# Kernel optimization log

Measured on AMD Instinct MI355X. Metric: run time of the kernel, lower is better.

## Reference

```python
import jax, jax.numpy as jnp
import numpy as np

N_NODES = 100000
N_EDGES = 1600000
IN_CH = 64
HID = 64
OUT_CH = 2
N_LAYERS = 3
NUM_GRAPHS = 2048
BN_EPS = 1e-5


def setup_inputs() -> dict:
    key = jax.random.key(0)
    ks = jax.random.split(key, 16)
    x = jax.random.normal(ks[0], (N_NODES, IN_CH), dtype=jnp.float32)
    edge_index = jax.random.randint(ks[1], (2, N_EDGES), 0, N_NODES, dtype=jnp.int32)
    batch = jnp.sort(jax.random.randint(ks[2], (N_NODES,), 0, NUM_GRAPHS, dtype=jnp.int32))
    s = 0.1  # weight scale
    inp = {
        "x": x,
        "edge_index": edge_index,
        "batch": batch,
        # stacked GINConv MLP params (in_ch == hidden so all layers share shapes)
        "convW1": jax.random.normal(ks[3], (N_LAYERS, IN_CH, HID), dtype=jnp.float32) * s,
        "convb1": jax.random.normal(ks[4], (N_LAYERS, HID), dtype=jnp.float32) * s,
        "bn_gamma": jnp.ones((N_LAYERS, HID), dtype=jnp.float32),
        "bn_beta": jnp.zeros((N_LAYERS, HID), dtype=jnp.float32),
        "bn_mean": jax.random.normal(ks[5], (N_LAYERS, HID), dtype=jnp.float32) * s,
        "bn_var": jax.random.uniform(ks[6], (N_LAYERS, HID), dtype=jnp.float32) + 0.5,
        "convW2": jax.random.normal(ks[7], (N_LAYERS, HID, HID), dtype=jnp.float32) * s,
        "convb2": jax.random.normal(ks[8], (N_LAYERS, HID), dtype=jnp.float32) * s,
        # final classifier MLP (norm=None, dropout=0.5 -> identity in eval)
        "mlpW1": jax.random.normal(ks[9], (HID, HID), dtype=jnp.float32) * s,
        "mlpb1": jax.random.normal(ks[10], (HID,), dtype=jnp.float32) * s,
        "mlpW2": jax.random.normal(ks[11], (HID, OUT_CH), dtype=jnp.float32) * s,
        "mlpb2": jax.random.normal(ks[12], (OUT_CH,), dtype=jnp.float32) * s,
    }
    return inp


def reference(x, edge_index, batch, convW1, convb1, bn_gamma, bn_beta, bn_mean,
              bn_var, convW2, convb2, mlpW1, mlpb1, mlpW2, mlpb2):
    N = x.shape[0]
    src, dst = edge_index[0], edge_index[1]
    for l in range(N_LAYERS):
        # GINConv, eps=0: h_i = MLP(x_i + sum_{j->i} x_j)
        agg = jax.ops.segment_sum(x[src], dst, num_segments=N)  # [N, C]
        h = x + agg
        # MLP: Linear -> BatchNorm(eval) -> ReLU -> Linear
        h = h @ convW1[l] + convb1[l]
        h = (h - bn_mean[l]) * jax.lax.rsqrt(bn_var[l] + BN_EPS) * bn_gamma[l] + bn_beta[l]
        h = jax.nn.relu(h)
        h = h @ convW2[l] + convb2[l]
        x = jax.nn.relu(h)  # .relu() after each conv in forward
    # global mean pool over graphs
    sums = jax.ops.segment_sum(x, batch, num_segments=NUM_GRAPHS)          # [G, H]
    counts = jax.ops.segment_sum(jnp.ones((N, 1), x.dtype), batch, num_segments=NUM_GRAPHS)
    pooled = sums / jnp.maximum(counts, 1.0)
    # final MLP: Linear -> ReLU -> (Dropout, identity in eval) -> Linear
    h = jax.nn.relu(pooled @ mlpW1 + mlpb1)
    logits = h @ mlpW2 + mlpb2
    return jax.nn.softmax(logits, axis=1)
```

## Files before the change

kernel.cpp:

```cpp
#include <hip/hip_runtime.h>

#define N_NODES   100000
#define N_EDGES   1600000
#define CH        64
#define N_LAYERS  3
#define NUM_GRAPHS 2048
#define BN_EPS    1e-5f
#define NSLICE    8
#define SLICE_SZ  12500

#define NP        100096
#define NBLK1     391
#define LDSTRIDE  65

__global__ __launch_bounds__(256) void hist_kernel(
    const int* __restrict__ dst, int* __restrict__ deg)
{
    int e = blockIdx.x * 256 + threadIdx.x;
    if (e < N_EDGES) atomicAdd(&deg[dst[e]], 1);
}

__global__ __launch_bounds__(256) void scan1_kernel(
    const int* __restrict__ deg, int* __restrict__ rowptr, int* __restrict__ blockSums)
{
    __shared__ int tmp[256];
    int t = threadIdx.x;
    int i = blockIdx.x * 256 + t;
    int v = (i < N_NODES) ? deg[i] : 0;
    tmp[t] = v;
    __syncthreads();
    for (int off = 1; off < 256; off <<= 1) {
        int a = (t >= off) ? tmp[t - off] : 0;
        __syncthreads();
        tmp[t] += a;
        __syncthreads();
    }
    if (i < N_NODES) rowptr[i] = tmp[t] - v;
    if (t == 255) blockSums[blockIdx.x] = tmp[255];
}

__global__ __launch_bounds__(512) void scan2_kernel(
    const int* __restrict__ blockSums, int* __restrict__ blockPrefix)
{
    __shared__ int tmp[512];
    int t = threadIdx.x;
    int v = (t < NBLK1) ? blockSums[t] : 0;
    tmp[t] = v;
    __syncthreads();
    for (int off = 1; off < 512; off <<= 1) {
        int a = (t >= off) ? tmp[t - off] : 0;
        __syncthreads();
        tmp[t] += a;
        __syncthreads();
    }
    if (t < NBLK1) blockPrefix[t] = tmp[t] - v;
}

__global__ __launch_bounds__(256) void scan3_kernel(
    int* __restrict__ rowptr, const int* __restrict__ blockPrefix)
{
    int i = blockIdx.x * 256 + threadIdx.x;
    if (i < N_NODES) rowptr[i] += blockPrefix[blockIdx.x];
}

__global__ __launch_bounds__(256) void scatter_edges_kernel(
    const int* __restrict__ src, const int* __restrict__ dst,
    int* __restrict__ rowptr, int* __restrict__ eidx)
{
    const int grp = blockIdx.x & (NSLICE - 1);
    const int ib  = blockIdx.x >> 3;
    const int nbx = gridDim.x >> 3;
    const int lo  = grp * SLICE_SZ;
    const int hi  = lo + SLICE_SZ;
    for (int e = ib * 256 + threadIdx.x; e < N_EDGES; e += nbx * 256) {
        int d = dst[e];
        if (d >= lo && d < hi) {
            int pos = atomicAdd(&rowptr[d], 1);
            eidx[pos] = src[e];
        }
    }
}

__global__ __launch_bounds__(256) void aggregate_kernel(
    const float* __restrict__ xin,
    const int*   __restrict__ rowptr, const int* __restrict__ deg,
    const int*   __restrict__ eidx,
    float*       __restrict__ h)
{
    int tid = blockIdx.x * 256 + threadIdx.x;
    int n  = tid >> 4;
    int cg = tid & 15;

    const float4* xv = (const float4*)xin;
    float4 acc = xv[(size_t)n * 16 + cg];

    int end = rowptr[n];
    int e   = end - deg[n];
    for (; e + 8 <= end; e += 8) {
        int s0 = eidx[e + 0], s1 = eidx[e + 1], s2 = eidx[e + 2], s3 = eidx[e + 3];
        int s4 = eidx[e + 4], s5 = eidx[e + 5], s6 = eidx[e + 6], s7 = eidx[e + 7];
        float4 a0 = xv[(size_t)s0 * 16 + cg];
        float4 a1 = xv[(size_t)s1 * 16 + cg];
        float4 a2 = xv[(size_t)s2 * 16 + cg];
        float4 a3 = xv[(size_t)s3 * 16 + cg];
        float4 a4 = xv[(size_t)s4 * 16 + cg];
        float4 a5 = xv[(size_t)s5 * 16 + cg];
        float4 a6 = xv[(size_t)s6 * 16 + cg];
        float4 a7 = xv[(size_t)s7 * 16 + cg];
        acc.x += a0.x; acc.y += a0.y; acc.z += a0.z; acc.w += a0.w;
        acc.x += a1.x; acc.y += a1.y; acc.z += a1.z; acc.w += a1.w;
        acc.x += a2.x; acc.y += a2.y; acc.z += a2.z; acc.w += a2.w;
        acc.x += a3.x; acc.y += a3.y; acc.z += a3.z; acc.w += a3.w;
        acc.x += a4.x; acc.y += a4.y; acc.z += a4.z; acc.w += a4.w;
        acc.x += a5.x; acc.y += a5.y; acc.z += a5.z; acc.w += a5.w;
        acc.x += a6.x; acc.y += a6.y; acc.z += a6.z; acc.w += a6.w;
        acc.x += a7.x; acc.y += a7.y; acc.z += a7.z; acc.w += a7.w;
    }
    for (; e + 4 <= end; e += 4) {
        int s0 = eidx[e + 0], s1 = eidx[e + 1], s2 = eidx[e + 2], s3 = eidx[e + 3];
        float4 a0 = xv[(size_t)s0 * 16 + cg];
        float4 a1 = xv[(size_t)s1 * 16 + cg];
        float4 a2 = xv[(size_t)s2 * 16 + cg];
        float4 a3 = xv[(size_t)s3 * 16 + cg];
        acc.x += a0.x; acc.y += a0.y; acc.z += a0.z; acc.w += a0.w;
        acc.x += a1.x; acc.y += a1.y; acc.z += a1.z; acc.w += a1.w;
        acc.x += a2.x; acc.y += a2.y; acc.z += a2.z; acc.w += a2.w;
        acc.x += a3.x; acc.y += a3.y; acc.z += a3.z; acc.w += a3.w;
    }
    for (; e < end; ++e) {
        float4 a = xv[(size_t)eidx[e] * 16 + cg];
        acc.x += a.x; acc.y += a.y; acc.z += a.z; acc.w += a.w;
    }
    ((float4*)h)[(size_t)n * 16 + cg] = acc;
}

__global__ __launch_bounds__(128) void mlp_kernel(
    const float* __restrict__ hin,
    const float* __restrict__ W1,   const float* __restrict__ b1,
    const float* __restrict__ gamma,const float* __restrict__ beta,
    const float* __restrict__ mean, const float* __restrict__ var,
    const float* __restrict__ W2,   const float* __restrict__ b2,
    float* __restrict__ xout)
{
    __shared__ float sbuf[2 * 64 * LDSTRIDE];

    const int lane = threadIdx.x & 63;
    const int wv   = threadIdx.x >> 6;
    const int gw   = blockIdx.x * 2 + wv;
    float* lds = sbuf + wv * (64 * LDSTRIDE);

    const long long base = (long long)gw * 64 * CH;
    const long long totF = (long long)N_NODES * CH;

    const float4* gin4 = (const float4*)(hin + base);
    for (int i = lane; i < 1024; i += 64) {
        int fo = i * 4;
        float4 v = make_float4(0.f, 0.f, 0.f, 0.f);
        if (base + fo + 3 < totF) v = gin4[i];
        int row = fo >> 6, col = fo & 63;
        float* p = lds + row * LDSTRIDE + col;
        p[0] = v.x; p[1] = v.y; p[2] = v.z; p[3] = v.w;
    }
    __syncthreads();

    float* myrow = lds + lane * LDSTRIDE;

    float a[CH];
    #pragma unroll
    for (int j = 0; j < CH; ++j) a[j] = b1[j];
    for (int k = 0; k < CH; ++k) {
        float hk = myrow[k];
        const float* wrow = W1 + k * CH;
        #pragma unroll
        for (int j = 0; j < CH; ++j)
            a[j] = fmaf(hk, wrow[j], a[j]);
    }

    #pragma unroll
    for (int j = 0; j < CH; ++j) {
        float sc = gamma[j] * rsqrtf(var[j] + BN_EPS);
        float sh = beta[j] - mean[j] * sc;
        myrow[j] = fmaxf(fmaf(a[j], sc, sh), 0.0f);
    }

    float c[CH];
    #pragma unroll
    for (int j = 0; j < CH; ++j) c[j] = b2[j];
    for (int k = 0; k < CH; ++k) {
        float tk = myrow[k];
        const float* wrow = W2 + k * CH;
        #pragma unroll
        for (int j = 0; j < CH; ++j)
            c[j] = fmaf(tk, wrow[j], c[j]);
    }

    #pragma unroll
    for (int j = 0; j < CH; ++j)
        myrow[j] = fmaxf(c[j], 0.0f);
    __syncthreads();

    float4* gout4 = (float4*)(xout + base);
    for (int i = lane; i < 1024; i += 64) {
        int fo = i * 4;
        if (base + fo + 3 < totF) {
            int row = fo >> 6, col = fo & 63;
            const float* p = lds + row * LDSTRIDE + col;
            gout4[i] = make_float4(p[0], p[1], p[2], p[3]);
        }
    }
}

__global__ __launch_bounds__(256) void pool_head_kernel(
    const float* __restrict__ x, const int* __restrict__ batch,
    const float* __restrict__ W1, const float* __restrict__ b1,
    const float* __restrict__ W2, const float* __restrict__ b2,
    float* __restrict__ out)
{
    __shared__ float w1[CH * CH];
    __shared__ float b1s[CH];
    __shared__ float w2s[CH * 2];

    for (int i = threadIdx.x; i < CH * CH; i += blockDim.x) w1[i] = W1[i];
    if (threadIdx.x < CH)     b1s[threadIdx.x] = b1[threadIdx.x];
    if (threadIdx.x < CH * 2) w2s[threadIdx.x] = W2[threadIdx.x];
    __syncthreads();

    const int lane = threadIdx.x & 63;
    const int g = blockIdx.x * (blockDim.x >> 6) + (threadIdx.x >> 6);
    if (g >= NUM_GRAPHS) return;

    int lo = 0, hi = N_NODES;
    while (lo < hi) { int mid = (lo + hi) >> 1; if (batch[mid] < g) lo = mid + 1; else hi = mid; }
    int start = lo;
    lo = start; hi = N_NODES;
    while (lo < hi) { int mid = (lo + hi) >> 1; if (batch[mid] < g + 1) lo = mid + 1; else hi = mid; }
    int end = lo;

    float s = 0.0f;
    for (int n = start; n < end; ++n) s += x[(size_t)n * CH + lane];
    int c = end - start;
    float p = s / (float)(c > 0 ? c : 1);

    float acc = b1s[lane];
    #pragma unroll
    for (int k = 0; k < CH; ++k)
        acc = fmaf(__shfl(p, k, 64), w1[k * CH + lane], acc);
    float h = fmaxf(acc, 0.0f);

    float l0 = h * w2s[lane * 2 + 0];
    float l1 = h * w2s[lane * 2 + 1];
    #pragma unroll
    for (int off = 32; off > 0; off >>= 1) {
        l0 += __shfl_xor(l0, off, 64);
        l1 += __shfl_xor(l1, off, 64);
    }
    if (lane == 0) {
        l0 += b2[0];
        l1 += b2[1];
        float m  = fmaxf(l0, l1);
        float e0 = expf(l0 - m), e1 = expf(l1 - m);
        float sm = e0 + e1;
        out[(size_t)g * 2 + 0] = e0 / sm;
        out[(size_t)g * 2 + 1] = e1 / sm;
    }
}

extern "C" void kernel_launch(void* const* d_in, const int* in_sizes, int n_in,
                              void* d_out, int out_size, void* d_ws, size_t ws_size,
                              hipStream_t stream)
{
    const float* x      = (const float*)d_in[0];
    const int*   ei     = (const int*)  d_in[1];
    const int*   src    = ei;
    const int*   dst    = ei + N_EDGES;
    const int*   batch  = (const int*)  d_in[2];
    const float* convW1 = (const float*)d_in[3];
    const float* convb1 = (const float*)d_in[4];
    const float* gamma  = (const float*)d_in[5];
    const float* beta   = (const float*)d_in[6];
    const float* mean   = (const float*)d_in[7];
    const float* var    = (const float*)d_in[8];
    const float* convW2 = (const float*)d_in[9];
    const float* convb2 = (const float*)d_in[10];
    const float* mlpW1  = (const float*)d_in[11];
    const float* mlpb1  = (const float*)d_in[12];
    const float* mlpW2  = (const float*)d_in[13];
    const float* mlpb2  = (const float*)d_in[14];
    float* out = (float*)d_out;

    int* deg         = (int*)d_ws;
    int* rowptr      = deg + NP;
    int* blockSums   = rowptr + NP;
    int* blockPrefix = blockSums + 512;
    int* eidx        = blockPrefix + 512;
    float* xA        = (float*)(eidx + N_EDGES);
    float* xB        = xA + (size_t)N_NODES * CH;

    hipMemsetAsync(deg, 0, NP * sizeof(int), stream);
    hist_kernel<<<(N_EDGES + 255) / 256, 256, 0, stream>>>(dst, deg);
    scan1_kernel<<<NBLK1, 256, 0, stream>>>(deg, rowptr, blockSums);
    scan2_kernel<<<1, 512, 0, stream>>>(blockSums, blockPrefix);
    scan3_kernel<<<NBLK1, 256, 0, stream>>>(rowptr, blockPrefix);
    scatter_edges_kernel<<<2048, 256, 0, stream>>>(src, dst, rowptr, eidx);

    const int aggGrid = (N_NODES * 16) / 256;
    const int mlpGrid = (N_NODES + 127) / 128;

    aggregate_kernel<<<aggGrid, 256, 0, stream>>>(x, rowptr, deg, eidx, xA);
    mlp_kernel<<<mlpGrid, 128, 0, stream>>>(xA,
        convW1, convb1, gamma, beta, mean, var, convW2, convb2, xA);
    aggregate_kernel<<<aggGrid, 256, 0, stream>>>(xA, rowptr, deg, eidx, xB);
    mlp_kernel<<<mlpGrid, 128, 0, stream>>>(xB,
        convW1 + CH*CH, convb1 + CH, gamma + CH, beta + CH, mean + CH, var + CH,
        convW2 + CH*CH, convb2 + CH, xB);
    aggregate_kernel<<<aggGrid, 256, 0, stream>>>(xB, rowptr, deg, eidx, xA);
    mlp_kernel<<<mlpGrid, 128, 0, stream>>>(xA,
        convW1 + 2*CH*CH, convb1 + 2*CH, gamma + 2*CH, beta + 2*CH, mean + 2*CH,
        var + 2*CH, convW2 + 2*CH*CH, convb2 + 2*CH, xA);

    pool_head_kernel<<<NUM_GRAPHS / 4, 256, 0, stream>>>(
        xA, batch, mlpW1, mlpb1, mlpW2, mlpb2, out);
}
```

Measured before the change: 602.1 us.

## Fuse neighbor aggregation with GIN MLP into one per-layer kernel

Merges the aggregate and MLP kernels into a single per-layer kernel. Each block gathers 64 nodes' aggregated features into LDS, then four waves each compute 16 output columns of both linear layers. This drops the global round trip of the aggregated buffer and one launch per layer, in exchange for more barriers and the MLP being split across waves. The edge scatter is also split into two launches over halves of the edge range, which may change atomic contention or ordering.

```diff
diff --git a/kernel.cpp b/kernel.cpp
--- a/kernel.cpp
+++ b/kernel.cpp
@@ -63,16 +63,17 @@
     if (i < N_NODES) rowptr[i] += blockPrefix[blockIdx.x];
 }
 
-__global__ __launch_bounds__(256) void scatter_edges_kernel(
+__global__ __launch_bounds__(256) void scatter_edges_half_kernel(
     const int* __restrict__ src, const int* __restrict__ dst,
-    int* __restrict__ rowptr, int* __restrict__ eidx)
+    int* __restrict__ rowptr, int* __restrict__ eidx,
+    int eBegin, int eEnd)
 {
     const int grp = blockIdx.x & (NSLICE - 1);
     const int ib  = blockIdx.x >> 3;
     const int nbx = gridDim.x >> 3;
     const int lo  = grp * SLICE_SZ;
     const int hi  = lo + SLICE_SZ;
-    for (int e = ib * 256 + threadIdx.x; e < N_EDGES; e += nbx * 256) {
+    for (int e = eBegin + ib * 256 + threadIdx.x; e < eEnd; e += nbx * 256) {
         int d = dst[e];
         if (d >= lo && d < hi) {
             int pos = atomicAdd(&rowptr[d], 1);
@@ -81,131 +82,130 @@
     }
 }
 
-__global__ __launch_bounds__(256) void aggregate_kernel(
+__global__ __launch_bounds__(256) void gin_layer_kernel(
     const float* __restrict__ xin,
     const int*   __restrict__ rowptr, const int* __restrict__ deg,
     const int*   __restrict__ eidx,
-    float*       __restrict__ h)
-{
-    int tid = blockIdx.x * 256 + threadIdx.x;
-    int n  = tid >> 4;
-    int cg = tid & 15;
-
-    const float4* xv = (const float4*)xin;
-    float4 acc = xv[(size_t)n * 16 + cg];
-
-    int end = rowptr[n];
-    int e   = end - deg[n];
-    for (; e + 8 <= end; e += 8) {
-        int s0 = eidx[e + 0], s1 = eidx[e + 1], s2 = eidx[e + 2], s3 = eidx[e + 3];
-        int s4 = eidx[e + 4], s5 = eidx[e + 5], s6 = eidx[e + 6], s7 = eidx[e + 7];
-        float4 a0 = xv[(size_t)s0 * 16 + cg];
-        float4 a1 = xv[(size_t)s1 * 16 + cg];
-        float4 a2 = xv[(size_t)s2 * 16 + cg];
-        float4 a3 = xv[(size_t)s3 * 16 + cg];
-        float4 a4 = xv[(size_t)s4 * 16 + cg];
-        float4 a5 = xv[(size_t)s5 * 16 + cg];
-        float4 a6 = xv[(size_t)s6 * 16 + cg];
-        float4 a7 = xv[(size_t)s7 * 16 + cg];
-        acc.x += a0.x; acc.y += a0.y; acc.z += a0.z; acc.w += a0.w;
-        acc.x += a1.x; acc.y += a1.y; acc.z += a1.z; acc.w += a1.w;
-        acc.x += a2.x; acc.y += a2.y; acc.z += a2.z; acc.w += a2.w;
-        acc.x += a3.x; acc.y += a3.y; acc.z += a3.z; acc.w += a3.w;
-        acc.x += a4.x; acc.y += a4.y; acc.z += a4.z; acc.w += a4.w;
-        acc.x += a5.x; acc.y += a5.y; acc.z += a5.z; acc.w += a5.w;
-        acc.x += a6.x; acc.y += a6.y; acc.z += a6.z; acc.w += a6.w;
-        acc.x += a7.x; acc.y += a7.y; acc.z += a7.z; acc.w += a7.w;
-    }
-    for (; e + 4 <= end; e += 4) {
-        int s0 = eidx[e + 0], s1 = eidx[e + 1], s2 = eidx[e + 2], s3 = eidx[e + 3];
-        float4 a0 = xv[(size_t)s0 * 16 + cg];
-        float4 a1 = xv[(size_t)s1 * 16 + cg];
-        float4 a2 = xv[(size_t)s2 * 16 + cg];
-        float4 a3 = xv[(size_t)s3 * 16 + cg];
-        acc.x += a0.x; acc.y += a0.y; acc.z += a0.z; acc.w += a0.w;
-        acc.x += a1.x; acc.y += a1.y; acc.z += a1.z; acc.w += a1.w;
-        acc.x += a2.x; acc.y += a2.y; acc.z += a2.z; acc.w += a2.w;
-        acc.x += a3.x; acc.y += a3.y; acc.z += a3.z; acc.w += a3.w;
-    }
-    for (; e < end; ++e) {
-        float4 a = xv[(size_t)eidx[e] * 16 + cg];
-        acc.x += a.x; acc.y += a.y; acc.z += a.z; acc.w += a.w;
-    }
-    ((float4*)h)[(size_t)n * 16 + cg] = acc;
-}
-
-__global__ __launch_bounds__(128) void mlp_kernel(
-    const float* __restrict__ hin,
     const float* __restrict__ W1,   const float* __restrict__ b1,
     const float* __restrict__ gamma,const float* __restrict__ beta,
     const float* __restrict__ mean, const float* __restrict__ var,
     const float* __restrict__ W2,   const float* __restrict__ b2,
     float* __restrict__ xout)
 {
-    __shared__ float sbuf[2 * 64 * LDSTRIDE];
-
-    const int lane = threadIdx.x & 63;
-    const int wv   = threadIdx.x >> 6;
-    const int gw   = blockIdx.x * 2 + wv;
-    float* lds = sbuf + wv * (64 * LDSTRIDE);
-
-    const long long base = (long long)gw * 64 * CH;
-    const long long totF = (long long)N_NODES * CH;
-
-    const float4* gin4 = (const float4*)(hin + base);
-    for (int i = lane; i < 1024; i += 64) {
-        int fo = i * 4;
-        float4 v = make_float4(0.f, 0.f, 0.f, 0.f);
-        if (base + fo + 3 < totF) v = gin4[i];
-        int row = fo >> 6, col = fo & 63;
-        float* p = lds + row * LDSTRIDE + col;
-        p[0] = v.x; p[1] = v.y; p[2] = v.z; p[3] = v.w;
-    }
-    __syncthreads();
-
-    float* myrow = lds + lane * LDSTRIDE;
-
-    float a[CH];
-    #pragma unroll
-    for (int j = 0; j < CH; ++j) a[j] = b1[j];
+    __shared__ float lh[64 * LDSTRIDE];
+
+    const int tid  = threadIdx.x;
+    const int lane = tid & 63;
+    const int wq   = tid >> 6;
+    const int nodeBase = blockIdx.x * 64;
+
+    const float4* xv = (const float4*)xin;
+
+    {
+        const int sub = tid >> 4;
+        const int cg  = tid & 15;
+        #pragma unroll
+        for (int p = 0; p < 4; ++p) {
+            int nl = p * 16 + sub;
+            int n  = nodeBase + nl;
+            if (n < N_NODES) {
+                float4 acc = xv[(size_t)n * 16 + cg];
+                int end = rowptr[n];
+                int e   = end - deg[n];
+                for (; e + 8 <= end; e += 8) {
+                    int s0 = eidx[e+0], s1 = eidx[e+1], s2 = eidx[e+2], s3 = eidx[e+3];
+                    int s4 = eidx[e+4], s5 = eidx[e+5], s6 = eidx[e+6], s7 = eidx[e+7];
+                    float4 a0 = xv[(size_t)s0 * 16 + cg];
+                    float4 a1 = xv[(size_t)s1 * 16 + cg];
+                    float4 a2 = xv[(size_t)s2 * 16 + cg];
+                    float4 a3 = xv[(size_t)s3 * 16 + cg];
+                    float4 a4 = xv[(size_t)s4 * 16 + cg];
+                    float4 a5 = xv[(size_t)s5 * 16 + cg];
+                    float4 a6 = xv[(size_t)s6 * 16 + cg];
+                    float4 a7 = xv[(size_t)s7 * 16 + cg];
+                    acc.x += a0.x; acc.y += a0.y; acc.z += a0.z; acc.w += a0.w;
+                    acc.x += a1.x; acc.y += a1.y; acc.z += a1.z; acc.w += a1.w;
+                    acc.x += a2.x; acc.y += a2.y; acc.z += a2.z; acc.w += a2.w;
+                    acc.x += a3.x; acc.y += a3.y; acc.z += a3.z; acc.w += a3.w;
+                    acc.x += a4.x; acc.y += a4.y; acc.z += a4.z; acc.w += a4.w;
+                    acc.x += a5.x; acc.y += a5.y; acc.z += a5.z; acc.w += a5.w;
+                    acc.x += a6.x; acc.y += a6.y; acc.z += a6.z; acc.w += a6.w;
+                    acc.x += a7.x; acc.y += a7.y; acc.z += a7.z; acc.w += a7.w;
+                }
+                for (; e + 4 <= end; e += 4) {
+                    int s0 = eidx[e+0], s1 = eidx[e+1], s2 = eidx[e+2], s3 = eidx[e+3];
+                    float4 a0 = xv[(size_t)s0 * 16 + cg];
+                    float4 a1 = xv[(size_t)s1 * 16 + cg];
+                    float4 a2 = xv[(size_t)s2 * 16 + cg];
+                    float4 a3 = xv[(size_t)s3 * 16 + cg];
+                    acc.x += a0.x; acc.y += a0.y; acc.z += a0.z; acc.w += a0.w;
+                    acc.x += a1.x; acc.y += a1.y; acc.z += a1.z; acc.w += a1.w;
+                    acc.x += a2.x; acc.y += a2.y; acc.z += a2.z; acc.w += a2.w;
+                    acc.x += a3.x; acc.y += a3.y; acc.z += a3.z; acc.w += a3.w;
+                }
+                for (; e < end; ++e) {
+                    float4 a = xv[(size_t)eidx[e] * 16 + cg];
+                    acc.x += a.x; acc.y += a.y; acc.z += a.z; acc.w += a.w;
+                }
+                float* pr = lh + nl * LDSTRIDE + cg * 4;
+                pr[0] = acc.x; pr[1] = acc.y; pr[2] = acc.z; pr[3] = acc.w;
+            }
+        }
+    }
+    __syncthreads();
+
+    const int j0 = wq * 16;
+    float* myrow = lh + lane * LDSTRIDE;
+
+    float a[16];
+    #pragma unroll
+    for (int jj = 0; jj < 16; ++jj) a[jj] = b1[j0 + jj];
     for (int k = 0; k < CH; ++k) {
         float hk = myrow[k];
-        const float* wrow = W1 + k * CH;
+        const float* wrow = W1 + k * CH + j0;
         #pragma unroll
-        for (int j = 0; j < CH; ++j)
-            a[j] = fmaf(hk, wrow[j], a[j]);
-    }
-
-    #pragma unroll
-    for (int j = 0; j < CH; ++j) {
-        float sc = gamma[j] * rsqrtf(var[j] + BN_EPS);
-        float sh = beta[j] - mean[j] * sc;
-        myrow[j] = fmaxf(fmaf(a[j], sc, sh), 0.0f);
-    }
-
-    float c[CH];
-    #pragma unroll
-    for (int j = 0; j < CH; ++j) c[j] = b2[j];
+        for (int jj = 0; jj < 16; ++jj)
+            a[jj] = fmaf(hk, wrow[jj], a[jj]);
+    }
+    __syncthreads();
+
+    #pragma unroll
+    for (int jj = 0; jj < 16; ++jj) {
+        float sc = gamma[j0 + jj] * rsqrtf(var[j0 + jj] + BN_EPS);
+        float sh = beta[j0 + jj] - mean[j0 + jj] * sc;
+        myrow[j0 + jj] = fmaxf(fmaf(a[jj], sc, sh), 0.0f);
+    }
+    __syncthreads();
+
+    float c[16];
+    #pragma unroll
+    for (int jj = 0; jj < 16; ++jj) c[jj] = b2[j0 + jj];
     for (int k = 0; k < CH; ++k) {
         float tk = myrow[k];
-        const float* wrow = W2 + k * CH;
+        const float* wrow = W2 + k * CH + j0;
         #pragma unroll
-        for (int j = 0; j < CH; ++j)
-            c[j] = fmaf(tk, wrow[j], c[j]);
-    }
-
-    #pragma unroll
-    for (int j = 0; j < CH; ++j)
-        myrow[j] = fmaxf(c[j], 0.0f);
-    __syncthreads();
-
-    float4* gout4 = (float4*)(xout + base);
-    for (int i = lane; i < 1024; i += 64) {
-        int fo = i * 4;
-        if (base + fo + 3 < totF) {
-            int row = fo >> 6, col = fo & 63;
-            const float* p = lds + row * LDSTRIDE + col;
-            gout4[i] = make_float4(p[0], p[1], p[2], p[3]);
+        for (int jj = 0; jj < 16; ++jj)
+            c[jj] = fmaf(tk, wrow[jj], c[jj]);
+    }
+    __syncthreads();
+
+    #pragma unroll
+    for (int jj = 0; jj < 16; ++jj)
+        myrow[j0 + jj] = fmaxf(c[jj], 0.0f);
+    __syncthreads();
+
+    {
+        const int sub = tid >> 4;
+        const int cg  = tid & 15;
+        float4* gout = (float4*)(xout + (size_t)nodeBase * CH);
+        #pragma unroll
+        for (int p = 0; p < 4; ++p) {
+            int nl = p * 16 + sub;
+            int n  = nodeBase + nl;
+            if (n < N_NODES) {
+                const float* pr = lh + nl * LDSTRIDE + cg * 4;
+                gout[nl * 16 + cg] = make_float4(pr[0], pr[1], pr[2], pr[3]);
+            }
         }
     }
 }
@@ -301,20 +301,19 @@
     scan1_kernel<<<NBLK1, 256, 0, stream>>>(deg, rowptr, blockSums);
     scan2_kernel<<<1, 512, 0, stream>>>(blockSums, blockPrefix);
     scan3_kernel<<<NBLK1, 256, 0, stream>>>(rowptr, blockPrefix);
-    scatter_edges_kernel<<<2048, 256, 0, stream>>>(src, dst, rowptr, eidx);
-
-    const int aggGrid = (N_NODES * 16) / 256;
-    const int mlpGrid = (N_NODES + 127) / 128;
-
-    aggregate_kernel<<<aggGrid, 256, 0, stream>>>(x, rowptr, deg, eidx, xA);
-    mlp_kernel<<<mlpGrid, 128, 0, stream>>>(xA,
+    scatter_edges_half_kernel<<<2048, 256, 0, stream>>>(src, dst, rowptr, eidx,
+                                                        0, N_EDGES / 2);
+    scatter_edges_half_kernel<<<2048, 256, 0, stream>>>(src, dst, rowptr, eidx,
+                                                        N_EDGES / 2, N_EDGES);
+
+    const int layerGrid = (N_NODES + 63) / 64;
+
+    gin_layer_kernel<<<layerGrid, 256, 0, stream>>>(x, rowptr, deg, eidx,
         convW1, convb1, gamma, beta, mean, var, convW2, convb2, xA);
-    aggregate_kernel<<<aggGrid, 256, 0, stream>>>(xA, rowptr, deg, eidx, xB);
-    mlp_kernel<<<mlpGrid, 128, 0, stream>>>(xB,
+    gin_layer_kernel<<<layerGrid, 256, 0, stream>>>(xA, rowptr, deg, eidx,
         convW1 + CH*CH, convb1 + CH, gamma + CH, beta + CH, mean + CH, var + CH,
         convW2 + CH*CH, convb2 + CH, xB);
-    aggregate_kernel<<<aggGrid, 256, 0, stream>>>(xB, rowptr, deg, eidx, xA);
-    mlp_kernel<<<mlpGrid, 128, 0, stream>>>(xA,
+    gin_layer_kernel<<<layerGrid, 256, 0, stream>>>(xB, rowptr, deg, eidx,
         convW1 + 2*CH*CH, convb1 + 2*CH, gamma + 2*CH, beta + 2*CH, mean + 2*CH,
         var + 2*CH, convW2 + 2*CH*CH, convb2 + 2*CH, xA);
 
```

Result: slower. 755.2 us (+25.4%).
